# Kernel optimization log

Measured on AMD Instinct MI355X. Metric: run time of the kernel, lower is better.

The kernel has to match this reference:

```python
import jax, jax.numpy as jnp
import numpy as np

N = 30000   # fluid particles
E = 480000  # edges
F = 4       # fluidFeatures (in channels)
P = 8       # RBF basis size per dim (dims=[8], 1D)
LAYERS = [32, 64, 64, 2]


def hat_basis(x, n):
    # 'linear' RBF: hat functions on n evenly spaced centers in [-1, 1]
    centers = jnp.linspace(-1.0, 1.0, n, dtype=x.dtype)
    spacing = 2.0 / (n - 1)
    return jnp.maximum(0.0, 1.0 - jnp.abs(x[:, None] - centers[None, :]) / spacing)  # [E, n]


def rbf_conv(x, fi, fj, d, W, b, mask, n_nodes):
    # x: [N, Cin]; d: [E, 1] clamped; W: [P, Cin, Cout]; b: [Cout]
    phi = hat_basis(d[:, 0], W.shape[0])      # [E, P]
    xj = x[fj]                                 # gather source features [E, Cin]
    msg = jnp.zeros((xj.shape[0], W.shape[2]), dtype=x.dtype)
    for p in range(W.shape[0]):                # small fixed P=8 loop keeps memory O(E*Cout)
        msg = msg + phi[:, p, None] * (xj @ W[p])
    msg = jnp.where(mask[:, None], msg, 0.0)   # centerIgnore: drop self edges fi==fj
    out = jax.ops.segment_sum(msg, fi, num_segments=n_nodes)  # scatter-reduce to targets
    return out + b


def _xavier(key, shape_in, shape_out):
    lim = float(np.sqrt(6.0 / (shape_in + shape_out)))
    return jax.random.uniform(key, (shape_in, shape_out), jnp.float32, -lim, lim)


def setup_inputs() -> dict:
    key = jax.random.key(0)
    ks = jax.random.split(key, 16)
    fluidFeatures = jax.random.normal(ks[0], (N, F), jnp.float32)
    fi = jax.random.randint(ks[1], (E,), 0, N)
    fj = jax.random.randint(ks[2], (E,), 0, N)
    distances = jax.random.normal(ks[3], (E, 1), jnp.float32)
    # conv channels: 4->32, 64->64, 64->64, 64->2
    cio = [(F, 32), (2 * 32, 64), (64, 64), (64, 2)]
    inp = {"fluidFeatures": fluidFeatures, "fi": fi, "fj": fj, "distances": distances}
    for li, (ci, co) in enumerate(cio):
        inp[f"cW{li}"] = jax.random.normal(ks[4 + li], (P, ci, co), jnp.float32) * (1.0 / np.sqrt(P * ci))
        inp[f"cb{li}"] = jnp.zeros((co,), jnp.float32)
        inp[f"fW{li}"] = _xavier(ks[8 + li], ci, co)   # stored [in, out]
        inp[f"fb{li}"] = jnp.zeros((co,), jnp.float32)
    return inp


def reference(fluidFeatures, fi, fj, distances,
              cW0, cb0, fW0, fb0, cW1, cb1, fW1, fb1,
              cW2, cb2, fW2, fb2, cW3, cb3, fW3, fb3):
    n_nodes = fluidFeatures.shape[0]
    mask = fi != fj                     # centerIgnore (mask instead of filter: jit-safe)
    d = jnp.clip(distances, -1.0, 1.0)

    conv0 = rbf_conv(fluidFeatures, fi, fj, d, cW0, cb0, mask, n_nodes)  # [N, 32]
    lin0 = fluidFeatures @ fW0 + fb0                                      # [N, 32]
    ans = jnp.concatenate([lin0, conv0], axis=1)                          # [N, 64]

    # i = 1: features[0]=32 != features[1]=64 -> no residual
    ansc = jax.nn.relu(ans)
    ans = rbf_conv(ansc, fi, fj, d, cW1, cb1, mask, n_nodes) + (ansc @ fW1 + fb1)
    # i = 2: features[1]==features[2]==64 and shapes match -> residual
    ansc = jax.nn.relu(ans)
    ans = rbf_conv(ansc, fi, fj, d, cW2, cb2, mask, n_nodes) + (ansc @ fW2 + fb2) + ans
    # i = 3: 64 -> 2, no residual
    ansc = jax.nn.relu(ans)
    ans = rbf_conv(ansc, fi, fj, d, cW3, cb3, mask, n_nodes) + (ansc @ fW3 + fb3)

    return ans  # dim == 1 (dims=[8]) -> no /128
```

## Files before the change

kernel.cpp:

```cpp
#include <hip/hip_runtime.h>


#define CAP 48

typedef __attribute__((ext_vector_type(8))) short short8;
typedef __attribute__((ext_vector_type(4))) short short4v;
typedef __attribute__((ext_vector_type(4))) float f32x4;

__device__ __forceinline__ short bf16s(float f) {
  unsigned u = __float_as_uint(f);
  return (short)((u + 0x7FFF + ((u >> 16) & 1)) >> 16);
}
__device__ __forceinline__ float b2f(unsigned short s) {
  return __uint_as_float(((unsigned)s) << 16);
}

__global__ void fill_prep(const float* __restrict__ dist,
                          const int* __restrict__ fi, const int* __restrict__ fj,
                          int* __restrict__ cnt, int* __restrict__ jw, int nE,
                          const float* __restrict__ cW1, const float* __restrict__ fW1,
                          const float* __restrict__ cW2, const float* __restrict__ fW2,
                          short* __restrict__ wt1, short* __restrict__ wt2,
                          const float* __restrict__ X,
                          const float* __restrict__ cW0,
                          const float* __restrict__ fW0,
                          unsigned short* __restrict__ U0, int n,
                          int fillBlocks, int prepBlocks) {
  if ((int)blockIdx.x < fillBlocks) {
    int e = blockIdx.x * blockDim.x + threadIdx.x;
    if (e >= nE) return;
    int i = fi[e], j = fj[e];
    if (i == j) return;
    float d = fminf(1.0f, fmaxf(-1.0f, dist[e]));
    float u = (d + 1.0f) * 3.5f;
    int p = min((int)u, 6);
    float w0 = 1.0f - (u - (float)p);
    int wq = (int)(w0 * 16383.0f + 0.5f);
    int pos = atomicAdd(&cnt[i], 1);
    if (pos < CAP)
      jw[(size_t)i * CAP + pos] = j | (p << 15) | (wq << 18);
  } else if ((int)blockIdx.x < fillBlocks + prepBlocks) {
    int idx = ((int)blockIdx.x - fillBlocks) * blockDim.x + threadIdx.x;
    if (idx >= 2 * 576 * 64) return;
    int sel = idx / (576 * 64);
    int r = idx - sel * (576 * 64);
    int col = r >> 6, ch = r & 63;
    const float* cW = sel ? cW2 : cW1;
    const float* fW = sel ? fW2 : fW1;
    float v;
    if (col < 512) {
      int p = col >> 6, co = col & 63;
      v = cW[((size_t)p * 64 + ch) * 64 + co];
    } else {
      v = fW[(size_t)ch * 64 + (col - 512)];
    }
    (sel ? wt2 : wt1)[(size_t)col * 64 + ch] = bf16s(v);
  } else {
    int idx = ((int)blockIdx.x - fillBlocks - prepBlocks) * blockDim.x + threadIdx.x;
    if (idx >= n * 288) return;
    int i = idx / 288, c = idx - i * 288;
    const float* x = X + (size_t)i * 4;
    float s = 0.0f;
    if (c < 256) {
      int p = c >> 5, co = c & 31;
      #pragma unroll
      for (int k = 0; k < 4; ++k) s = fmaf(x[k], cW0[((size_t)p * 4 + k) * 32 + co], s);
    } else {
      int co = c - 256;
      #pragma unroll
      for (int k = 0; k < 4; ++k) s = fmaf(x[k], fW0[(size_t)k * 32 + co], s);
    }
    U0[(size_t)i * 288 + c] = (unsigned short)bf16s(s);
  }
}

__global__ __launch_bounds__(1024) void layer0_gemm(
    const unsigned short* __restrict__ U0,
    const int* __restrict__ cnt, const int* __restrict__ jw,
    const float* __restrict__ cb0, const float* __restrict__ fb0,
    const short* __restrict__ WTul,
    unsigned short* __restrict__ UL, int n) {
  __shared__ __align__(16) unsigned short sXa[16 * 64];
  __shared__ __align__(16) short sUL[16 * 584];
  const int tid = threadIdx.x;
  const int w = tid >> 6;
  const int lane = tid & 63;
  const int grp = lane >> 5;
  const int gl = lane & 31;
  const int nodeBase = blockIdx.x * 16;
  const int i = nodeBase + w;
  const bool valid = (i < n);
  const int ic = valid ? i : 0;

  int rec = jw[(size_t)ic * CAP + (lane < CAP ? lane : 0)];
  const int m = valid ? min(cnt[ic], CAP) : 0;
  const int mc = m - 1;
  float accLo = 0.0f, accHi = 0.0f;
  for (int q0 = 0; q0 < m; q0 += 16) {
    unsigned raw[8];
    float ws[8];
    #pragma unroll
    for (int k = 0; k < 8; ++k) {
      int eA = q0 + 2 * k;
      int vA = __builtin_amdgcn_readlane(rec, min(eA, mc));
      int vB = __builtin_amdgcn_readlane(rec, min(eA + 1, mc));
      int v = grp ? vB : vA;
      int j = v & 0x7FFF;
      int p = (v >> 15) & 7;
      float w0 = (float)((unsigned)v >> 18) * (1.0f / 16383.0f);
      float wgt = (gl < 16) ? w0 : (1.0f - w0);
      ws[k] = (eA + grp < m) ? wgt : 0.0f;
      raw[k] = ((const unsigned*)(U0 + (size_t)j * 288 + p * 32))[gl];
    }
    #pragma unroll
    for (int k = 0; k < 8; ++k) {
      accLo = fmaf(ws[k], __uint_as_float(raw[k] << 16), accLo);
      accHi = fmaf(ws[k], __uint_as_float(raw[k] & 0xFFFF0000u), accHi);
    }
  }
  accLo += __shfl_xor(accLo, 16, 64);
  accHi += __shfl_xor(accHi, 16, 64);
  accLo += __shfl_xor(accLo, 32, 64);
  accHi += __shfl_xor(accHi, 32, 64);
  if (lane < 16) {
    const int l = lane;
    float c0v = fmaxf(accLo + cb0[2 * l], 0.0f);
    float c1v = fmaxf(accHi + cb0[2 * l + 1], 0.0f);
    unsigned lr = ((const unsigned*)(U0 + (size_t)ic * 288 + 256))[l];
    float l0 = fmaxf(__uint_as_float(lr << 16) + fb0[2 * l], 0.0f);
    float l1 = fmaxf(__uint_as_float(lr & 0xFFFF0000u) + fb0[2 * l + 1], 0.0f);
    unsigned* row = (unsigned*)(sXa + w * 64);
    row[l] = (unsigned)(unsigned short)bf16s(l0) | ((unsigned)(unsigned short)bf16s(l1) << 16);
    row[16 + l] = (unsigned)(unsigned short)bf16s(c0v) | ((unsigned)(unsigned short)bf16s(c1v) << 16);
  }
  __syncthreads();

  const int mrow = lane & 15;
  const int quad = lane >> 4;
  short8 b0 = *(const short8*)(sXa + mrow * 64 + quad * 8);
  short8 b1 = *(const short8*)(sXa + mrow * 64 + quad * 8 + 32);
  for (int t = w; t < 36; t += 16) {
    const short* aBase = WTul + (size_t)(t * 16 + mrow) * 64 + quad * 8;
    short8 a0 = *(const short8*)(aBase);
    short8 a1 = *(const short8*)(aBase + 32);
    f32x4 acc = {0, 0, 0, 0};
    acc = __builtin_amdgcn_mfma_f32_16x16x32_bf16(a0, b0, acc, 0, 0, 0);
    acc = __builtin_amdgcn_mfma_f32_16x16x32_bf16(a1, b1, acc, 0, 0, 0);
    short4v pk;
    #pragma unroll
    for (int reg = 0; reg < 4; ++reg) pk[reg] = bf16s(acc[reg]);
    *(short4v*)(sUL + mrow * 584 + t * 16 + quad * 4) = pk;
  }
  __syncthreads();
  const int r = tid >> 6;
  const int c0 = tid & 63;
  if (nodeBase + r < n) {
    unsigned short* dst = UL + (size_t)(nodeBase + r) * 576;
    #pragma unroll
    for (int chunk = c0; chunk < 72; chunk += 64)
      *(short8*)(dst + chunk * 8) = *(const short8*)(sUL + r * 584 + chunk * 8);
  }
}

__global__ __launch_bounds__(256) void gemm_ul(
    const unsigned short* __restrict__ Xb,
    const short* __restrict__ WTul,
    unsigned short* __restrict__ UL, int n) {
  __shared__ short sUL[16 * 584];
  const int lane = threadIdx.x & 63;
  const int w = threadIdx.x >> 6;
  const int mrow = lane & 15;
  const int quad = lane >> 4;
  const int nodeBase = blockIdx.x * 16;
  const int bnode = min(nodeBase + mrow, n - 1);
  const unsigned short* bBase = Xb + (size_t)bnode * 64 + quad * 8;
  short8 b0 = *(const short8*)(bBase);
  short8 b1 = *(const short8*)(bBase + 32);
  #pragma unroll
  for (int t = 0; t < 9; ++t) {
    const int ct = w * 9 + t;
    const short* aBase = WTul + (size_t)(ct * 16 + mrow) * 64 + quad * 8;
    short8 a0 = *(const short8*)(aBase);
    short8 a1 = *(const short8*)(aBase + 32);
    f32x4 acc = {0, 0, 0, 0};
    acc = __builtin_amdgcn_mfma_f32_16x16x32_bf16(a0, b0, acc, 0, 0, 0);
    acc = __builtin_amdgcn_mfma_f32_16x16x32_bf16(a1, b1, acc, 0, 0, 0);
    short4v pk;
    #pragma unroll
    for (int reg = 0; reg < 4; ++reg) pk[reg] = bf16s(acc[reg]);
    *(short4v*)(sUL + mrow * 584 + ct * 16 + quad * 4) = pk;
  }
  __syncthreads();
  const int r = threadIdx.x >> 4;
  const int c0 = threadIdx.x & 15;
  if (nodeBase + r < n) {
    unsigned short* dst = UL + (size_t)(nodeBase + r) * 576;
    #pragma unroll
    for (int chunk = c0; chunk < 72; chunk += 16)
      *(short8*)(dst + chunk * 8) = *(const short8*)(sUL + r * 584 + chunk * 8);
  }
}

template <bool HAS_RES, bool STORE_ANS, bool COMPUTE_T>
__global__ __launch_bounds__(256) void conv_gather(
    const unsigned short* __restrict__ UL,
    const int* __restrict__ cnt, const int* __restrict__ jw,
    const float* __restrict__ cb, const float* __restrict__ fb,
    const float* __restrict__ resid,
    const float* __restrict__ cW3,
    float* __restrict__ T,
    float* __restrict__ outAns,
    unsigned short* __restrict__ outAnsc, int n) {
  const int lane = threadIdx.x & 63;
  const int half = lane >> 5;
  const int pl = lane & 31;
  const int i = (blockIdx.x * blockDim.x + threadIdx.x) >> 6;
  if (i >= n) return;
  int rec = jw[(size_t)i * CAP + (lane < CAP ? lane : 0)];
  const int m = min(cnt[i], CAP);
  const int mc = m - 1;
  const unsigned short* ULrow = UL + (size_t)i * 576;
  const unsigned Lraw = ((const unsigned*)(ULrow + 512))[pl];
  float rv0 = 0.0f, rv1 = 0.0f;
  if (HAS_RES) {
    float2 rv = *(const float2*)(resid + (size_t)i * 64 + 2 * pl);
    rv0 = rv.x; rv1 = rv.y;
  }
  float accLo = 0.0f, accHi = 0.0f;
  for (int q0 = 0; q0 < m; q0 += 16) {
    unsigned raw[16];
    float w0s[16];
    #pragma unroll
    for (int k = 0; k < 16; ++k) {
      int v = __builtin_amdgcn_readlane(rec, min(q0 + k, mc));
      int j = v & 0x7FFF;
      int p = (v >> 15) & 7;
      w0s[k] = (float)((unsigned)v >> 18) * (1.0f / 16383.0f);
      raw[k] = ((const unsigned*)(UL + (size_t)j * 576 + p * 64))[lane];
    }
    #pragma unroll
    for (int k = 0; k < 16; ++k) {
      bool ok = (q0 + k < m);
      float w = half ? (1.0f - w0s[k]) : w0s[k];
      w = ok ? w : 0.0f;
      accLo = fmaf(w, __uint_as_float(raw[k] << 16), accLo);
      accHi = fmaf(w, __uint_as_float(raw[k] & 0xFFFF0000u), accHi);
    }
  }
  accLo += __shfl_xor(accLo, 32, 64);
  accHi += __shfl_xor(accHi, 32, 64);
  if (half == 0) {
    const int c0i = 2 * pl, c1i = c0i + 1;
    float L0 = __uint_as_float(Lraw << 16);
    float L1 = __uint_as_float(Lraw & 0xFFFF0000u);
    float o0 = accLo + L0 + cb[c0i] + fb[c0i] + rv0;
    float o1 = accHi + L1 + cb[c1i] + fb[c1i] + rv1;
    if (STORE_ANS)
      *(float2*)(outAns + (size_t)i * 64 + c0i) = make_float2(o0, o1);
    unsigned short xb0 = (unsigned short)bf16s(fmaxf(o0, 0.0f));
    unsigned short xb1 = (unsigned short)bf16s(fmaxf(o1, 0.0f));
    ((unsigned*)(outAnsc + (size_t)i * 64))[pl] = (unsigned)xb0 | ((unsigned)xb1 << 16);
    if (COMPUTE_T) {
      float x0 = b2f(xb0), x1 = b2f(xb1);
      float c[16];
      #pragma unroll
      for (int t = 0; t < 16; ++t) {
        const float* wrow = cW3 + ((size_t)(t >> 1) * 64) * 2 + (t & 1);
        c[t] = x0 * wrow[c0i * 2] + x1 * wrow[c1i * 2];
      }
      #pragma unroll
      for (int off = 16; off > 0; off >>= 1) {
        #pragma unroll
        for (int t = 0; t < 16; ++t) c[t] += __shfl_xor(c[t], off, 64);
      }
      if (pl == 0) {
        float* tr = T + (size_t)i * 16;
        #pragma unroll
        for (int t = 0; t < 16; ++t) tr[t] = c[t];
      }
    }
  }
}

__global__ __launch_bounds__(256, 4) void layer3_kernel(
    const unsigned short* __restrict__ Xb,
    const float* __restrict__ T,
    const int* __restrict__ cnt, const int* __restrict__ jw,
    const float* __restrict__ cb3, const float* __restrict__ fb3,
    const float* __restrict__ fW3,
    float* __restrict__ out, int n) {
  const int lane = threadIdx.x & 63;
  const int i = (blockIdx.x * blockDim.x + threadIdx.x) >> 6;
  if (i >= n) return;
  const int m = min(cnt[i], CAP);
  float c0 = 0.0f, c1 = 0.0f;
  if (lane < m) {
    int v = jw[(size_t)i * CAP + lane];
    int j = min(v & 0x7FFF, n - 1);
    int p = (v >> 15) & 7;
    float w0 = (float)((unsigned)v >> 18) * (1.0f / 16383.0f);
    float w1 = 1.0f - w0;
    const float* tb = T + (size_t)j * 16 + p * 2;
    float2 ta = *(const float2*)(tb);
    float2 tc = *(const float2*)(tb + 2);
    c0 = w0 * ta.x + w1 * tc.x;
    c1 = w0 * ta.y + w1 * tc.y;
  }
  float xi = b2f(Xb[(size_t)i * 64 + lane]);
  float2 fw = *(const float2*)(fW3 + lane * 2);
  c0 = fmaf(xi, fw.x, c0);
  c1 = fmaf(xi, fw.y, c1);
  #pragma unroll
  for (int off = 32; off > 0; off >>= 1) {
    c0 += __shfl_xor(c0, off, 64);
    c1 += __shfl_xor(c1, off, 64);
  }
  if (lane == 0) {
    out[(size_t)i * 2 + 0] = c0 + cb3[0] + fb3[0];
    out[(size_t)i * 2 + 1] = c1 + cb3[1] + fb3[1];
  }
}

extern "C" void kernel_launch(void* const* d_in, const int* in_sizes, int n_in,
                              void* d_out, int out_size, void* d_ws, size_t ws_size,
                              hipStream_t stream) {
  const float* X    = (const float*)d_in[0];
  const int*   fi   = (const int*)d_in[1];
  const int*   fj   = (const int*)d_in[2];
  const float* dist = (const float*)d_in[3];
  const float* cW0 = (const float*)d_in[4];  const float* cb0 = (const float*)d_in[5];
  const float* fW0 = (const float*)d_in[6];  const float* fb0 = (const float*)d_in[7];
  const float* cW1 = (const float*)d_in[8];  const float* cb1 = (const float*)d_in[9];
  const float* fW1 = (const float*)d_in[10]; const float* fb1 = (const float*)d_in[11];
  const float* cW2 = (const float*)d_in[12]; const float* cb2 = (const float*)d_in[13];
  const float* fW2 = (const float*)d_in[14]; const float* fb2 = (const float*)d_in[15];
  const float* cW3 = (const float*)d_in[16]; const float* cb3 = (const float*)d_in[17];
  const float* fW3 = (const float*)d_in[18]; const float* fb3 = (const float*)d_in[19];
  float* out = (float*)d_out;

  const int n  = in_sizes[0] / 4;
  const int nE = in_sizes[1];

  unsigned short* UL    = (unsigned short*)d_ws;
  unsigned short* ansc2 = UL + (size_t)n * 576;
  unsigned short* ansc1 = ansc2 + (size_t)n * 64;
  float*          ans1  = (float*)(ansc1 + (size_t)n * 64);
  float* T     = ans1 + (size_t)n * 64;
  short* wtul1 = (short*)(T + (size_t)n * 16);
  short* wtul2 = wtul1 + 576 * 64;
  int*   jw    = (int*)(wtul2 + 576 * 64);
  int*   cnt   = jw + (size_t)n * CAP;
  unsigned short* U0 = (unsigned short*)(cnt + n);

  hipMemsetAsync(cnt, 0, (size_t)n * sizeof(int), stream);
  const int fillBlocks = (nE + 255) / 256;
  const int prepBlocks = (2 * 576 * 64 + 255) / 256;
  const int u0Blocks   = (n * 288 + 255) / 256;
  fill_prep<<<fillBlocks + prepBlocks + u0Blocks, 256, 0, stream>>>(
      dist, fi, fj, cnt, jw, nE, cW1, fW1, cW2, fW2, wtul1, wtul2,
      X, cW0, fW0, U0, n, fillBlocks, prepBlocks);

  layer0_gemm<<<(n + 15) / 16, 1024, 0, stream>>>(U0, cnt, jw, cb0, fb0,
                                                  wtul1, UL, n);
  conv_gather<false, true, false><<<(n * 64 + 255) / 256, 256, 0, stream>>>(
      UL, cnt, jw, cb1, fb1, nullptr, nullptr, nullptr, ans1, ansc1, n);
  gemm_ul<<<(n + 15) / 16, 256, 0, stream>>>(ansc1, wtul2, UL, n);
  conv_gather<true, false, true><<<(n * 64 + 255) / 256, 256, 0, stream>>>(
      UL, cnt, jw, cb2, fb2, ans1, cW3, T, nullptr, ansc2, n);
  layer3_kernel<<<(n * 64 + 255) / 256, 256, 0, stream>>>(ansc2, T, cnt, jw,
                                                          cb3, fb3, fW3, out, n);
}
```

Before: 261.2 us.

## Fuse layer-1 gather with layer-2 projection GEMM and vectorize U0 prep

```diff
diff --git a/kernel.cpp b/kernel.cpp
--- a/kernel.cpp
+++ b/kernel.cpp
@@ -13,6 +13,9 @@
 }
 __device__ __forceinline__ float b2f(unsigned short s) {
   return __uint_as_float(((unsigned)s) << 16);
+}
+__device__ __forceinline__ unsigned pack2(float a, float b) {
+  return (unsigned)(unsigned short)bf16s(a) | ((unsigned)(unsigned short)bf16s(b) << 16);
 }
 
 __global__ void fill_prep(const float* __restrict__ dist,
@@ -57,20 +60,31 @@
     (sel ? wt2 : wt1)[(size_t)col * 64 + ch] = bf16s(v);
   } else {
     int idx = ((int)blockIdx.x - fillBlocks - prepBlocks) * blockDim.x + threadIdx.x;
-    if (idx >= n * 288) return;
-    int i = idx / 288, c = idx - i * 288;
-    const float* x = X + (size_t)i * 4;
-    float s = 0.0f;
-    if (c < 256) {
-      int p = c >> 5, co = c & 31;
+    if (idx >= n * 72) return;
+    int i = idx / 72, g = idx - i * 72;
+    float4 x = *(const float4*)(X + (size_t)i * 4);
+    float xk[4] = {x.x, x.y, x.z, x.w};
+    float s[4] = {0, 0, 0, 0};
+    if (g < 64) {
+      int p = g >> 3;
+      int co = (g * 4) & 31;
       #pragma unroll
-      for (int k = 0; k < 4; ++k) s = fmaf(x[k], cW0[((size_t)p * 4 + k) * 32 + co], s);
+      for (int k = 0; k < 4; ++k) {
+        const float* wr = cW0 + ((size_t)p * 4 + k) * 32 + co;
+        #pragma unroll
+        for (int c = 0; c < 4; ++c) s[c] = fmaf(xk[k], wr[c], s[c]);
+      }
     } else {
-      int co = c - 256;
+      int co = (g - 64) * 4;
       #pragma unroll
-      for (int k = 0; k < 4; ++k) s = fmaf(x[k], fW0[(size_t)k * 32 + co], s);
-    }
-    U0[(size_t)i * 288 + c] = (unsigned short)bf16s(s);
+      for (int k = 0; k < 4; ++k) {
+        const float* wr = fW0 + (size_t)k * 32 + co;
+        #pragma unroll
+        for (int c = 0; c < 4; ++c) s[c] = fmaf(xk[k], wr[c], s[c]);
+      }
+    }
+    uint2 pk = make_uint2(pack2(s[0], s[1]), pack2(s[2], s[3]));
+    *(uint2*)(U0 + (size_t)i * 288 + g * 4) = pk;
   }
 }
 
@@ -130,8 +144,8 @@
     float l0 = fmaxf(__uint_as_float(lr << 16) + fb0[2 * l], 0.0f);
     float l1 = fmaxf(__uint_as_float(lr & 0xFFFF0000u) + fb0[2 * l + 1], 0.0f);
     unsigned* row = (unsigned*)(sXa + w * 64);
-    row[l] = (unsigned)(unsigned short)bf16s(l0) | ((unsigned)(unsigned short)bf16s(l1) << 16);
-    row[16 + l] = (unsigned)(unsigned short)bf16s(c0v) | ((unsigned)(unsigned short)bf16s(c1v) << 16);
+    row[l] = pack2(l0, l1);
+    row[16 + l] = pack2(c0v, c1v);
   }
   __syncthreads();
 
@@ -162,24 +176,72 @@
   }
 }
 
-__global__ __launch_bounds__(256) void gemm_ul(
-    const unsigned short* __restrict__ Xb,
-    const short* __restrict__ WTul,
-    unsigned short* __restrict__ UL, int n) {
-  __shared__ short sUL[16 * 584];
-  const int lane = threadIdx.x & 63;
-  const int w = threadIdx.x >> 6;
+__global__ __launch_bounds__(1024) void conv_gemm(
+    const unsigned short* __restrict__ ULA,
+    const int* __restrict__ cnt, const int* __restrict__ jw,
+    const float* __restrict__ cb, const float* __restrict__ fb,
+    const short* __restrict__ WTul2,
+    float* __restrict__ outAns,
+    unsigned short* __restrict__ ULB, int n) {
+  __shared__ __align__(16) unsigned short sXa[16 * 64];
+  __shared__ __align__(16) short sUL[16 * 584];
+  const int tid = threadIdx.x;
+  const int w = tid >> 6;
+  const int lane = tid & 63;
+  const int half = lane >> 5;
+  const int pl = lane & 31;
+  const int nodeBase = blockIdx.x * 16;
+  const int i = nodeBase + w;
+  const bool valid = (i < n);
+  const int ic = valid ? i : 0;
+
+  int rec = jw[(size_t)ic * CAP + (lane < CAP ? lane : 0)];
+  const int m = valid ? min(cnt[ic], CAP) : 0;
+  const int mc = m - 1;
+  const unsigned Lraw = ((const unsigned*)(ULA + (size_t)ic * 576 + 512))[pl];
+  float accLo = 0.0f, accHi = 0.0f;
+  for (int q0 = 0; q0 < m; q0 += 16) {
+    unsigned raw[16];
+    float w0s[16];
+    #pragma unroll
+    for (int k = 0; k < 16; ++k) {
+      int v = __builtin_amdgcn_readlane(rec, min(q0 + k, mc));
+      int j = v & 0x7FFF;
+      int p = (v >> 15) & 7;
+      w0s[k] = (float)((unsigned)v >> 18) * (1.0f / 16383.0f);
+      raw[k] = ((const unsigned*)(ULA + (size_t)j * 576 + p * 64))[lane];
+    }
+    #pragma unroll
+    for (int k = 0; k < 16; ++k) {
+      bool ok = (q0 + k < m);
+      float wv = half ? (1.0f - w0s[k]) : w0s[k];
+      wv = ok ? wv : 0.0f;
+      accLo = fmaf(wv, __uint_as_float(raw[k] << 16), accLo);
+      accHi = fmaf(wv, __uint_as_float(raw[k] & 0xFFFF0000u), accHi);
+    }
+  }
+  accLo += __shfl_xor(accLo, 32, 64);
+  accHi += __shfl_xor(accHi, 32, 64);
+  if (half == 0) {
+    unsigned* row = (unsigned*)(sXa + w * 64);
+    if (valid) {
+      const int c0i = 2 * pl, c1i = c0i + 1;
+      float o0 = accLo + __uint_as_float(Lraw << 16) + cb[c0i] + fb[c0i];
+      float o1 = accHi + __uint_as_float(Lraw & 0xFFFF0000u) + cb[c1i] + fb[c1i];
+      *(float2*)(outAns + (size_t)i * 64 + c0i) = make_float2(o0, o1);
+      row[pl] = pack2(fmaxf(o0, 0.0f), fmaxf(o1, 0.0f));
+    } else {
+      row[pl] = 0u;
+    }
+  }
+  __syncthreads();
+
   const int mrow = lane & 15;
   const int quad = lane >> 4;
-  const int nodeBase = blockIdx.x * 16;
-  const int bnode = min(nodeBase + mrow, n - 1);
-  const unsigned short* bBase = Xb + (size_t)bnode * 64 + quad * 8;
-  short8 b0 = *(const short8*)(bBase);
-  short8 b1 = *(const short8*)(bBase + 32);
-  #pragma unroll
-  for (int t = 0; t < 9; ++t) {
-    const int ct = w * 9 + t;
-    const short* aBase = WTul + (size_t)(ct * 16 + mrow) * 64 + quad * 8;
+  short8 b0 = *(const short8*)(sXa + mrow * 64 + quad * 8);
+  short8 b1 = *(const short8*)(sXa + mrow * 64 + quad * 8 + 32);
+  for (int t = w; t < 36; t += 16) {
+    const short* aBase = WTul2 + (size_t)(t * 16 + mrow) * 64 + quad * 8;
     short8 a0 = *(const short8*)(aBase);
     short8 a1 = *(const short8*)(aBase + 32);
     f32x4 acc = {0, 0, 0, 0};
@@ -188,28 +250,26 @@
     short4v pk;
     #pragma unroll
     for (int reg = 0; reg < 4; ++reg) pk[reg] = bf16s(acc[reg]);
-    *(short4v*)(sUL + mrow * 584 + ct * 16 + quad * 4) = pk;
+    *(short4v*)(sUL + mrow * 584 + t * 16 + quad * 4) = pk;
   }
   __syncthreads();
-  const int r = threadIdx.x >> 4;
-  const int c0 = threadIdx.x & 15;
+  const int r = tid >> 6;
+  const int c0 = tid & 63;
   if (nodeBase + r < n) {
-    unsigned short* dst = UL + (size_t)(nodeBase + r) * 576;
-    #pragma unroll
-    for (int chunk = c0; chunk < 72; chunk += 16)
+    unsigned short* dst = ULB + (size_t)(nodeBase + r) * 576;
+    #pragma unroll
+    for (int chunk = c0; chunk < 72; chunk += 64)
       *(short8*)(dst + chunk * 8) = *(const short8*)(sUL + r * 584 + chunk * 8);
   }
 }
 
-template <bool HAS_RES, bool STORE_ANS, bool COMPUTE_T>
-__global__ __launch_bounds__(256) void conv_gather(
+__global__ __launch_bounds__(256) void conv2_kernel(
     const unsigned short* __restrict__ UL,
     const int* __restrict__ cnt, const int* __restrict__ jw,
     const float* __restrict__ cb, const float* __restrict__ fb,
     const float* __restrict__ resid,
     const float* __restrict__ cW3,
     float* __restrict__ T,
-    float* __restrict__ outAns,
     unsigned short* __restrict__ outAnsc, int n) {
   const int lane = threadIdx.x & 63;
   const int half = lane >> 5;
@@ -219,13 +279,8 @@
   int rec = jw[(size_t)i * CAP + (lane < CAP ? lane : 0)];
   const int m = min(cnt[i], CAP);
   const int mc = m - 1;
-  const unsigned short* ULrow = UL + (size_t)i * 576;
-  const unsigned Lraw = ((const unsigned*)(ULrow + 512))[pl];
-  float rv0 = 0.0f, rv1 = 0.0f;
-  if (HAS_RES) {
-    float2 rv = *(const float2*)(resid + (size_t)i * 64 + 2 * pl);
-    rv0 = rv.x; rv1 = rv.y;
-  }
+  const unsigned Lraw = ((const unsigned*)(UL + (size_t)i * 576 + 512))[pl];
+  float2 rv = *(const float2*)(resid + (size_t)i * 64 + 2 * pl);
   float accLo = 0.0f, accHi = 0.0f;
   for (int q0 = 0; q0 < m; q0 += 16) {
     unsigned raw[16];
@@ -241,43 +296,37 @@
     #pragma unroll
     for (int k = 0; k < 16; ++k) {
       bool ok = (q0 + k < m);
-      float w = half ? (1.0f - w0s[k]) : w0s[k];
-      w = ok ? w : 0.0f;
-      accLo = fmaf(w, __uint_as_float(raw[k] << 16), accLo);
-      accHi = fmaf(w, __uint_as_float(raw[k] & 0xFFFF0000u), accHi);
+      float wv = half ? (1.0f - w0s[k]) : w0s[k];
+      wv = ok ? wv : 0.0f;
+      accLo = fmaf(wv, __uint_as_float(raw[k] << 16), accLo);
+      accHi = fmaf(wv, __uint_as_float(raw[k] & 0xFFFF0000u), accHi);
     }
   }
   accLo += __shfl_xor(accLo, 32, 64);
   accHi += __shfl_xor(accHi, 32, 64);
   if (half == 0) {
     const int c0i = 2 * pl, c1i = c0i + 1;
-    float L0 = __uint_as_float(Lraw << 16);
-    float L1 = __uint_as_float(Lraw & 0xFFFF0000u);
-    float o0 = accLo + L0 + cb[c0i] + fb[c0i] + rv0;
-    float o1 = accHi + L1 + cb[c1i] + fb[c1i] + rv1;
-    if (STORE_ANS)
-      *(float2*)(outAns + (size_t)i * 64 + c0i) = make_float2(o0, o1);
+    float o0 = accLo + __uint_as_float(Lraw << 16) + cb[c0i] + fb[c0i] + rv.x;
+    float o1 = accHi + __uint_as_float(Lraw & 0xFFFF0000u) + cb[c1i] + fb[c1i] + rv.y;
     unsigned short xb0 = (unsigned short)bf16s(fmaxf(o0, 0.0f));
     unsigned short xb1 = (unsigned short)bf16s(fmaxf(o1, 0.0f));
     ((unsigned*)(outAnsc + (size_t)i * 64))[pl] = (unsigned)xb0 | ((unsigned)xb1 << 16);
-    if (COMPUTE_T) {
-      float x0 = b2f(xb0), x1 = b2f(xb1);
-      float c[16];
+    float x0 = b2f(xb0), x1 = b2f(xb1);
+    float c[16];
+    #pragma unroll
+    for (int t = 0; t < 16; ++t) {
+      const float* wrow = cW3 + ((size_t)(t >> 1) * 64) * 2 + (t & 1);
+      c[t] = x0 * wrow[c0i * 2] + x1 * wrow[c1i * 2];
+    }
+    #pragma unroll
+    for (int off = 16; off > 0; off >>= 1) {
       #pragma unroll
-      for (int t = 0; t < 16; ++t) {
-        const float* wrow = cW3 + ((size_t)(t >> 1) * 64) * 2 + (t & 1);
-        c[t] = x0 * wrow[c0i * 2] + x1 * wrow[c1i * 2];
-      }
+      for (int t = 0; t < 16; ++t) c[t] += __shfl_xor(c[t], off, 64);
+    }
+    if (pl == 0) {
+      float* tr = T + (size_t)i * 16;
       #pragma unroll
-      for (int off = 16; off > 0; off >>= 1) {
-        #pragma unroll
-        for (int t = 0; t < 16; ++t) c[t] += __shfl_xor(c[t], off, 64);
-      }
-      if (pl == 0) {
-        float* tr = T + (size_t)i * 16;
-        #pragma unroll
-        for (int t = 0; t < 16; ++t) tr[t] = c[t];
-      }
+      for (int t = 0; t < 16; ++t) tr[t] = c[t];
     }
   }
 }
@@ -341,32 +390,31 @@
   const int n  = in_sizes[0] / 4;
   const int nE = in_sizes[1];
 
-  unsigned short* UL    = (unsigned short*)d_ws;
-  unsigned short* ansc2 = UL + (size_t)n * 576;
-  unsigned short* ansc1 = ansc2 + (size_t)n * 64;
-  float*          ans1  = (float*)(ansc1 + (size_t)n * 64);
-  float* T     = ans1 + (size_t)n * 64;
+  unsigned short* ULA   = (unsigned short*)d_ws;
+  unsigned short* ULB   = ULA + (size_t)n * 576;
+  unsigned short* U0    = ULB;
+  float*          ans1  = (float*)(ULB + (size_t)n * 576);
+  unsigned short* ansc2 = (unsigned short*)(ans1 + (size_t)n * 64);
+  float* T     = (float*)(ansc2 + (size_t)n * 64);
   short* wtul1 = (short*)(T + (size_t)n * 16);
   short* wtul2 = wtul1 + 576 * 64;
   int*   jw    = (int*)(wtul2 + 576 * 64);
   int*   cnt   = jw + (size_t)n * CAP;
-  unsigned short* U0 = (unsigned short*)(cnt + n);
 
   hipMemsetAsync(cnt, 0, (size_t)n * sizeof(int), stream);
   const int fillBlocks = (nE + 255) / 256;
   const int prepBlocks = (2 * 576 * 64 + 255) / 256;
-  const int u0Blocks   = (n * 288 + 255) / 256;
+  const int u0Blocks   = (n * 72 + 255) / 256;
   fill_prep<<<fillBlocks + prepBlocks + u0Blocks, 256, 0, stream>>>(
       dist, fi, fj, cnt, jw, nE, cW1, fW1, cW2, fW2, wtul1, wtul2,
       X, cW0, fW0, U0, n, fillBlocks, prepBlocks);
 
   layer0_gemm<<<(n + 15) / 16, 1024, 0, stream>>>(U0, cnt, jw, cb0, fb0,
-                                                  wtul1, UL, n);
-  conv_gather<false, true, false><<<(n * 64 + 255) / 256, 256, 0, stream>>>(
-      UL, cnt, jw, cb1, fb1, nullptr, nullptr, nullptr, ans1, ansc1, n);
-  gemm_ul<<<(n + 15) / 16, 256, 0, stream>>>(ansc1, wtul2, UL, n);
-  conv_gather<true, false, true><<<(n * 64 + 255) / 256, 256, 0, stream>>>(
-      UL, cnt, jw, cb2, fb2, ans1, cW3, T, nullptr, ansc2, n);
+                                                  wtul1, ULA, n);
+  conv_gemm<<<(n + 15) / 16, 1024, 0, stream>>>(ULA, cnt, jw, cb1, fb1,
+                                                wtul2, ans1, ULB, n);
+  conv2_kernel<<<(n * 64 + 255) / 256, 256, 0, stream>>>(
+      ULB, cnt, jw, cb2, fb2, ans1, cW3, T, ansc2, n);
   layer3_kernel<<<(n * 64 + 255) / 256, 256, 0, stream>>>(ansc2, T, cnt, jw,
                                                           cb3, fb3, fW3, out, n);
 }
```

New measurement: 250.0 us. -4.3%, faster.
